# Kernel tuning notes

Hardware: AMD Instinct MI355X
Metric: run time of the kernel (lower is better)

Reference implementation:

```python
import jax, jax.numpy as jnp
import numpy as np

HID = 2048      # hidden_size
NH = 16         # num_attention_heads
QLR = 1536      # q_lora_rank
KVLR = 512      # kv_lora_rank
DN = 128        # qk_nope_head_dim
DR = 64         # qk_rope_head_dim
DQK = DN + DR   # qk_head_dim = 192
DV = 128        # v_head_dim
EPS = 1e-6
THETA = 10000.0
B, T = 2, 2048


def rmsnorm(x, scale):
    return x * jax.lax.rsqrt(jnp.mean(x * x, axis=-1, keepdims=True) + EPS) * scale


def rope(x, positions):
    # x: [B, T, h, d]; NeoX-style rotate-half RoPE on the rope slice only
    d = x.shape[-1]
    inv_freq = 1.0 / (THETA ** (jnp.arange(0, d, 2, dtype=jnp.float32) / d))
    ang = positions.astype(jnp.float32)[..., None] * inv_freq       # [B, T, d/2]
    cos = jnp.cos(ang)[:, :, None, :]
    sin = jnp.sin(ang)[:, :, None, :]
    x1, x2 = jnp.split(x, 2, axis=-1)
    return jnp.concatenate([x1 * cos - x2 * sin, x2 * cos + x1 * sin], axis=-1).astype(x.dtype)


def setup_inputs() -> dict:
    key = jax.random.key(0)
    ks = jax.random.split(key, 8)
    s = 0.02
    x = jax.random.normal(ks[0], (B, T, HID), dtype=jnp.float32)
    attention_mask = jnp.ones((B, T), dtype=bool)
    positions = jnp.broadcast_to(jnp.arange(T, dtype=jnp.int32), (B, T))
    wqa = jax.random.normal(ks[1], (HID, QLR), dtype=jnp.float32) * s
    qa_scale = jnp.ones((QLR,), dtype=jnp.float32)
    wqb = jax.random.normal(ks[2], (QLR, NH * DQK), dtype=jnp.float32) * s
    wkva = jax.random.normal(ks[3], (HID, KVLR + DR), dtype=jnp.float32) * s
    kva_scale = jnp.ones((KVLR,), dtype=jnp.float32)
    wkvb = jax.random.normal(ks[4], (KVLR, NH * (DN + DV)), dtype=jnp.float32) * s
    wo = jax.random.normal(ks[5], (NH * DV, HID), dtype=jnp.float32) * s
    return {"x": x, "attention_mask": attention_mask, "positions": positions,
            "wqa": wqa, "qa_scale": qa_scale, "wqb": wqb,
            "wkva": wkva, "kva_scale": kva_scale, "wkvb": wkvb, "wo": wo}


def reference(x, attention_mask, positions, wqa, qa_scale, wqb, wkva, kva_scale, wkvb, wo):
    Bv, Tv, _ = x.shape
    # low-rank Q: hid -> q_lora_rank -> rmsnorm -> heads*qk_head_dim
    q = (rmsnorm(x @ wqa, qa_scale) @ wqb).reshape(Bv, Tv, NH, DQK)
    q_pass, q_rot = q[..., :DN], q[..., DN:]
    # compressed KV + shared rope key
    ckv = x @ wkva                                    # [B, T, KVLR + DR]
    kv_lat, k_rot = ckv[..., :KVLR], ckv[..., KVLR:].reshape(Bv, Tv, 1, DR)
    kv = (rmsnorm(kv_lat, kva_scale) @ wkvb).reshape(Bv, Tv, NH, DN + DV)
    k_pass, v = kv[..., :DN], kv[..., DN:]
    # decoupled RoPE on rope slice only
    q_rot = rope(q_rot, positions)
    k_rot = jnp.broadcast_to(rope(k_rot, positions), (Bv, Tv, NH, DR))
    q = jnp.concatenate([q_pass, q_rot], axis=-1)     # [B, T, H, 192]
    k = jnp.concatenate([k_pass, k_rot], axis=-1)
    # masked causal SDPA; v padding in the original is a no-op mathematically
    scale = DQK ** -0.5
    scores = jnp.einsum('bqhd,bkhd->bhqk', q, k) * scale
    causal = jnp.tril(jnp.ones((Tv, Tv), dtype=bool))
    mask = causal[None, None, :, :] & attention_mask[:, None, None, :].astype(bool)
    scores = jnp.where(mask, scores, jnp.finfo(scores.dtype).min)
    probs = jax.nn.softmax(scores, axis=-1)
    out = jnp.einsum('bhqk,bkhd->bqhd', probs, v).reshape(Bv, Tv, NH * DV)
    return out @ wo
```

## Files before the change

kernel.cpp:

```cpp
#include <hip/hip_runtime.h>
#include <math.h>
#include <stdint.h>

#define NHEAD 16
#define HIDDIM 2048
#define QLRANK 1536
#define KVRANK 512
#define DROT 64
#define BB 2
#define TT 2048
#define BTOK (BB*TT)
#define NPROJ 2176
#define CKV0 1536
#define ROT0 2048

typedef __bf16 bf16x8 __attribute__((ext_vector_type(8)));
typedef __bf16 bf16x4 __attribute__((ext_vector_type(4)));
typedef float f32x4 __attribute__((ext_vector_type(4)));
typedef uint16_t u16;

__device__ __forceinline__ u16 f2bf(float f) {
  union { float f; uint32_t u; } v; v.f = f;
  uint32_t r = v.u + 0x7fffu + ((v.u >> 16) & 1u);
  return (u16)(r >> 16);
}
__device__ __forceinline__ float bf2f(u16 h) {
  union { uint32_t u; float f; } v; v.u = ((uint32_t)h) << 16;
  return v.f;
}

__device__ __forceinline__ void gload_lds16(const u16* g, u16* l) {
  __builtin_amdgcn_global_load_lds(
      (const __attribute__((address_space(1))) uint32_t*)g,
      (__attribute__((address_space(3))) uint32_t*)l, 16, 0, 0);
}

__global__ __launch_bounds__(256) void cvt_f32_bf16(const float* __restrict__ in,
                                                    u16* __restrict__ out, int n) {
  int idx = (blockIdx.x * 256 + threadIdx.x) * 8;
  if (idx >= n) return;
  f32x4 a = *(const f32x4*)&in[idx];
  f32x4 b = *(const f32x4*)&in[idx + 4];
  union { f32x4 q; u16 e[8]; } w;
#pragma unroll
  for (int j = 0; j < 4; ++j) { w.e[j] = f2bf(a[j]); w.e[4 + j] = f2bf(b[j]); }
  *(f32x4*)&out[idx] = w.q;
}

__global__ __launch_bounds__(256) void transpose_w(const float* __restrict__ W,
                                                   u16* __restrict__ Wt,
                                                   int K, int N, int Npad, float scale,
                                                   const float* __restrict__ svec) {
  __shared__ float tile[32][33];
  int k0 = blockIdx.x * 32, n0 = blockIdx.y * 32;
  int tx = threadIdx.x, ty = threadIdx.y;
#pragma unroll
  for (int r = 0; r < 32; r += 8) {
    int k = k0 + ty + r, n = n0 + tx;
    tile[ty + r][tx] = (k < K && n < N) ? W[(size_t)k * N + n] : 0.f;
  }
  __syncthreads();
  float sv = scale * (svec ? svec[k0 + tx] : 1.f);
#pragma unroll
  for (int r = 0; r < 32; r += 8) {
    int n = n0 + ty + r, k = k0 + tx;
    if (n < Npad && k < K) Wt[(size_t)n * K + k] = f2bf(tile[tx][ty + r] * sv);
  }
}

template<int D>
__global__ __launch_bounds__(256) void row_invrms(const u16* __restrict__ in, int stride,
                                                  float* __restrict__ out) {
  const int row = blockIdx.x;
  const int tid = threadIdx.x;
  constexpr int NC = D / 8;
  float ss = 0.f;
  if (tid < NC) {
    union { f32x4 q; u16 e[8]; } t;
    t.q = *(const f32x4*)&in[(size_t)row * stride + tid * 8];
#pragma unroll
    for (int j = 0; j < 8; ++j) { float v = bf2f(t.e[j]); ss += v * v; }
  }
#pragma unroll
  for (int off = 1; off < 64; off <<= 1) ss += __shfl_xor(ss, off);
  __shared__ float red[4];
  if ((tid & 63) == 0) red[tid >> 6] = ss;
  __syncthreads();
  if (tid == 0)
    out[row] = rsqrtf((red[0] + red[1] + red[2] + red[3]) / (float)D + 1e-6f);
}

template<int OUTF32>
__global__ __launch_bounds__(256) void gemm_bt(const u16* __restrict__ A, int lda,
                                               const u16* __restrict__ Bt,
                                               void* __restrict__ Cv, int ldc,
                                               const float* __restrict__ rowscale,
                                               int N, int K) {
  __shared__ __align__(16) u16 As[2][128 * 32];
  __shared__ __align__(16) u16 Bs[2][128 * 32];
  const int tid = threadIdx.x;
  const int lane = tid & 63;
  const int wave = tid >> 6;
  const int bm = blockIdx.y * 128;
  const int bn = blockIdx.x * 128;
  const int wr = wave >> 1;
  const int wc = wave & 1;

  f32x4 acc[4][4] = {};

  const int srow = wave * 16 + (lane >> 2);
  const int scol = (lane & 3) * 8;
  const u16* Ag = A + (size_t)(bm + srow) * lda + scol;
  const u16* Bg = Bt + (size_t)(bn + srow) * K + scol;
  const int soff = (wave * 16) * 32;

  const int a_off = (wr * 64 + (lane & 15)) * 32 + (lane >> 4) * 8;
  const int b_off = (wc * 64 + (lane & 15)) * 32 + (lane >> 4) * 8;

  const int nt = K >> 5;

  gload_lds16(Ag, &As[0][soff]);
  gload_lds16(Ag + (size_t)64 * lda, &As[0][soff + 64 * 32]);
  gload_lds16(Bg, &Bs[0][soff]);
  gload_lds16(Bg + (size_t)64 * K, &Bs[0][soff + 64 * 32]);
  __syncthreads();

  int cur = 0;
  for (int t = 0; t < nt; ++t) {
    if (t + 1 < nt) {
      const int k0 = (t + 1) << 5;
      gload_lds16(Ag + k0, &As[cur ^ 1][soff]);
      gload_lds16(Ag + (size_t)64 * lda + k0, &As[cur ^ 1][soff + 64 * 32]);
      gload_lds16(Bg + k0, &Bs[cur ^ 1][soff]);
      gload_lds16(Bg + (size_t)64 * K + k0, &Bs[cur ^ 1][soff + 64 * 32]);
    }
    bf16x8 af[4], bfr[4];
#pragma unroll
    for (int m = 0; m < 4; ++m) af[m] = *(const bf16x8*)&As[cur][a_off + m * 16 * 32];
#pragma unroll
    for (int n = 0; n < 4; ++n) bfr[n] = *(const bf16x8*)&Bs[cur][b_off + n * 16 * 32];
#pragma unroll
    for (int m = 0; m < 4; ++m)
#pragma unroll
      for (int n = 0; n < 4; ++n)
        acc[m][n] = __builtin_amdgcn_mfma_f32_16x16x32_bf16(af[m], bfr[n], acc[m][n], 0, 0, 0);
    if (t + 1 < nt) {
      __syncthreads();
      cur ^= 1;
    }
  }

  const int row0 = bm + wr * 64 + (lane >> 4) * 4;
  const int col0 = bn + wc * 64 + (lane & 15);
#pragma unroll
  for (int m = 0; m < 4; ++m) {
    float rs[4] = {1.f, 1.f, 1.f, 1.f};
    if (rowscale) {
#pragma unroll
      for (int i = 0; i < 4; ++i) rs[i] = rowscale[row0 + m * 16 + i];
    }
#pragma unroll
    for (int n = 0; n < 4; ++n)
#pragma unroll
      for (int i = 0; i < 4; ++i) {
        size_t idx = (size_t)(row0 + m * 16 + i) * ldc + (col0 + n * 16);
        float v = acc[m][n][i] * rs[i];
        if (OUTF32) ((float*)Cv)[idx] = v;
        else        ((u16*)Cv)[idx] = f2bf(v);
      }
  }
}

__global__ __launch_bounds__(256) void rope_table(const int* __restrict__ positions,
                                                  float2* __restrict__ tab) {
  int idx = blockIdx.x * 256 + threadIdx.x;
  if (idx >= BTOK * 32) return;
  int bt = idx >> 5, i = idx & 31;
  float invf = powf(10000.0f, -(float)i / 32.0f);
  float ang = (float)positions[bt] * invf;
  tab[idx] = make_float2(cosf(ang), sinf(ang));
}

__global__ __launch_bounds__(256) void rope_q(u16* __restrict__ q,
                                              const float2* __restrict__ tab) {
  int idx = blockIdx.x * 256 + threadIdx.x;
  if (idx >= BTOK * NHEAD * 32) return;
  int i = idx & 31;
  int h = (idx >> 5) & 15;
  int bt = idx >> 9;
  u16* p = q + (size_t)bt * 3072 + h * 192 + 128;
  float x1 = bf2f(p[i]), x2 = bf2f(p[32 + i]);
  float2 cs = tab[bt * 32 + i];
  p[i] = f2bf(x1 * cs.x - x2 * cs.y);
  p[32 + i] = f2bf(x2 * cs.x + x1 * cs.y);
}

__global__ __launch_bounds__(256) void assemble_k(const u16* __restrict__ kv,
                                                  const u16* __restrict__ proj,
                                                  const float2* __restrict__ tab,
                                                  u16* __restrict__ kf) {
  int bt = blockIdx.x;
  __shared__ __align__(16) u16 krot[64];
  int t = threadIdx.x;
  if (t < 64) {
    int i = t & 31;
    float2 cs = tab[bt * 32 + i];
    float x1 = bf2f(proj[(size_t)bt * NPROJ + ROT0 + i]);
    float x2 = bf2f(proj[(size_t)bt * NPROJ + ROT0 + 32 + i]);
    krot[t] = f2bf((t < 32) ? (x1 * cs.x - x2 * cs.y) : (x2 * cs.x + x1 * cs.y));
  }
  __syncthreads();
  for (int c = t; c < 16 * 24; c += 256) {
    int h = c / 24, seg = c % 24;
    u16* dst = kf + (size_t)bt * 3072 + h * 192 + seg * 8;
    if (seg < 16)
      *(f32x4*)dst = *(const f32x4*)&kv[(size_t)bt * 4096 + h * 256 + seg * 8];
    else
      *(f32x4*)dst = *(const f32x4*)&krot[(seg - 16) * 8];
  }
}

__device__ const int8_t JOB_QT[24] = {15,15,7,14,14,13,13,6,12,12,11,11,5,10,10,9,9,4,8,8,3,2,1,0};
__device__ const int8_t JOB_PC[24] = { 0, 1,2, 0, 1, 0, 1,2, 0, 1, 0, 1,2, 0, 1,0,1,2,0,1,2,2,2,2};

__global__ __launch_bounds__(256, 2) void attn_fwd3(const u16* __restrict__ Q,
                                                    const u16* __restrict__ Kf,
                                                    const u16* __restrict__ KV,
                                                    u16* __restrict__ O,
                                                    u16* __restrict__ Opart,
                                                    float2* __restrict__ ml) {
  __shared__ __align__(16) u16 Ks[64 * 192];
  __shared__ __align__(16) u16 Vs[64 * 128];
  __shared__ __align__(16) u16 Ps[4][32][72];

  const int tid = threadIdx.x, lane = tid & 63, wave = tid >> 6;
  const int l15 = lane & 15, l4 = lane >> 4;
  const int jobrank = blockIdx.x >> 5;
  const int bh = blockIdx.x & 31;
  const int qt = JOB_QT[jobrank];
  const int piece = JOB_PC[jobrank];
  const int q0 = qt * 128;
  const int b = bh >> 4, h = bh & 15;
  const int wq0 = q0 + wave * 32;

  bf16x8 qf[2][6];
#pragma unroll
  for (int m = 0; m < 2; ++m) {
    const u16* qp = Q + (size_t)(b * TT + wq0 + m * 16 + l15) * 3072 + h * 192 + l4 * 8;
#pragma unroll
    for (int kk = 0; kk < 6; ++kk) qf[m][kk] = *(const bf16x8*)(qp + kk * 32);
  }

  int ksrc[6];
#pragma unroll
  for (int j = 0; j < 6; ++j) {
    int o = (wave * 6 + j) * 1024 + lane * 16;
    int row = o / 384, col = o % 384;
    int scol = col ^ ((row & 7) << 4);
    ksrc[j] = row * 3072 + (scol >> 1);
  }
  int vsrc[4];
#pragma unroll
  for (int j = 0; j < 4; ++j) {
    int lam = (wave * 4 + j) * 512 + lane * 8;
    int kap = ((lam >> 6) & 15) * 4 + ((lam >> 4) & 3);
    int key = (kap & 3) * 16 + (kap >> 5) * 8 + ((kap >> 2) & 7);
    int dv  = (lam >> 10) * 16 + (lam & 15);
    vsrc[j] = key * 4096 + dv;
  }
  const u16* Kbase = Kf + (size_t)(b * TT) * 3072 + h * 192;
  const u16* Vbase = KV + (size_t)(b * TT) * 4096 + h * 256 + 128;
  u16* KsW = Ks + (wave * 6) * 512;
  u16* VsW = Vs + (wave * 4) * 512;
  const unsigned vs_base = (unsigned)(uintptr_t)(&Vs[0]);

  f32x4 o_acc[2][8] = {};
  float m_r[2][4], l_r[2][4];
#pragma unroll
  for (int m = 0; m < 2; ++m)
#pragma unroll
    for (int i = 0; i < 4; ++i) { m_r[m][i] = -INFINITY; l_r[m][i] = 0.f; }

  const int kt0 = (piece == 1) ? (qt + 1) : 0;
  const int kt1 = (piece == 0) ? (qt + 1) : (2 * qt + 2);

  for (int kt = kt0; kt < kt1; ++kt) {
    __syncthreads();
    const u16* Kt = Kbase + (size_t)(kt * 64) * 3072;
    const u16* Vt = Vbase + (size_t)(kt * 64) * 4096;
#pragma unroll
    for (int j = 0; j < 6; ++j) gload_lds16(Kt + ksrc[j], KsW + j * 512);
#pragma unroll
    for (int j = 0; j < 4; ++j) gload_lds16(Vt + vsrc[j], VsW + j * 512);
    __syncthreads();

    if (kt * 64 > wq0 + 31) continue;

    f32x4 s[2][4] = {};
#pragma unroll
    for (int n = 0; n < 4; ++n) {
      const int krow = n * 16 + l15;
      const int swz = (l15 & 7) << 3;
#pragma unroll
      for (int kk = 0; kk < 6; ++kk) {
        bf16x8 kb = *(const bf16x8*)&Ks[krow * 192 + ((kk * 32 + l4 * 8) ^ swz)];
        s[0][n] = __builtin_amdgcn_mfma_f32_16x16x32_bf16(qf[0][kk], kb, s[0][n], 0, 0, 0);
        s[1][n] = __builtin_amdgcn_mfma_f32_16x16x32_bf16(qf[1][kk], kb, s[1][n], 0, 0, 0);
      }
    }

    const bool needmask = (kt * 64 + 63) > wq0;
    const int pbase = (l15 >> 3) * 32 + (l15 & 3) * 8 + ((l15 >> 2) & 1) * 4;
#pragma unroll
    for (int m = 0; m < 2; ++m) {
      float sv[4][4], pmax[4], alpha[4];
      const int qrow0 = wq0 + m * 16 + l4 * 4;
#pragma unroll
      for (int i = 0; i < 4; ++i) pmax[i] = -INFINITY;
#pragma unroll
      for (int n = 0; n < 4; ++n)
#pragma unroll
        for (int i = 0; i < 4; ++i) {
          float v = s[m][n][i];
          if (needmask && (kt * 64 + n * 16 + l15 > qrow0 + i)) v = -INFINITY;
          sv[n][i] = v;
          pmax[i] = fmaxf(pmax[i], v);
        }
#pragma unroll
      for (int i = 0; i < 4; ++i) {
#pragma unroll
        for (int off = 1; off < 16; off <<= 1) pmax[i] = fmaxf(pmax[i], __shfl_xor(pmax[i], off));
        float mn = fmaxf(m_r[m][i], pmax[i]);
        alpha[i] = __expf(m_r[m][i] - mn);
        m_r[m][i] = mn;
      }
      float psum[4] = {0.f, 0.f, 0.f, 0.f};
#pragma unroll
      for (int i = 0; i < 4; ++i) {
        union { uint2 d; u16 e[4]; } pk;
#pragma unroll
        for (int n = 0; n < 4; ++n) {
          float p = __expf(sv[n][i] - m_r[m][i]);
          psum[i] += p;
          pk.e[n] = f2bf(p);
        }
        *(uint2*)&Ps[wave][m * 16 + l4 * 4 + i][pbase] = pk.d;
      }
#pragma unroll
      for (int i = 0; i < 4; ++i) {
#pragma unroll
        for (int off = 1; off < 16; off <<= 1) psum[i] += __shfl_xor(psum[i], off);
        l_r[m][i] = l_r[m][i] * alpha[i] + psum[i];
      }
#pragma unroll
      for (int n = 0; n < 8; ++n)
#pragma unroll
        for (int i = 0; i < 4; ++i) o_acc[m][n][i] *= alpha[i];
    }

    asm volatile("s_waitcnt lgkmcnt(0)" ::: "memory");
    __builtin_amdgcn_sched_barrier(0);

#pragma unroll
    for (int kk = 0; kk < 2; ++kk) {
      bf16x8 pa0 = *(const bf16x8*)&Ps[wave][l15][kk * 32 + l4 * 8];
      bf16x8 pa1 = *(const bf16x8*)&Ps[wave][16 + l15][kk * 32 + l4 * 8];
      const unsigned va = vs_base + kk * 1024 + lane * 8;
#pragma unroll
      for (int g = 0; g < 2; ++g) {
        union { uint2 u; bf16x4 b; } lo[4], hi[4];
#pragma unroll
        for (int n = 0; n < 4; ++n) {
          unsigned a0 = va + (g * 4 + n) * 2048;
          asm volatile("ds_read_b64_tr_b16 %0, %1" : "=v"(lo[n].u) : "v"(a0));
          asm volatile("ds_read_b64_tr_b16 %0, %1 offset:512" : "=v"(hi[n].u) : "v"(a0));
        }
        asm volatile("s_waitcnt lgkmcnt(0)" ::: "memory");
        __builtin_amdgcn_sched_barrier(0);
#pragma unroll
        for (int n = 0; n < 4; ++n) {
          bf16x8 vb = __builtin_shufflevector(lo[n].b, hi[n].b, 0, 1, 2, 3, 4, 5, 6, 7);
          o_acc[0][g * 4 + n] = __builtin_amdgcn_mfma_f32_16x16x32_bf16(pa0, vb, o_acc[0][g * 4 + n], 0, 0, 0);
          o_acc[1][g * 4 + n] = __builtin_amdgcn_mfma_f32_16x16x32_bf16(pa1, vb, o_acc[1][g * 4 + n], 0, 0, 0);
        }
      }
    }
  }

  if (piece == 2) {
    float l_inv[2][4];
#pragma unroll
    for (int m = 0; m < 2; ++m)
#pragma unroll
      for (int i = 0; i < 4; ++i) l_inv[m][i] = 1.f / l_r[m][i];
#pragma unroll
    for (int m = 0; m < 2; ++m)
#pragma unroll
      for (int n = 0; n < 8; ++n)
#pragma unroll
        for (int i = 0; i < 4; ++i) {
          int r = q0 + wave * 32 + m * 16 + l4 * 4 + i;
          O[(size_t)(b * TT + r) * 2048 + h * 128 + n * 16 + l15] = f2bf(o_acc[m][n][i] * l_inv[m][i]);
        }
  } else {
    const size_t pidx = ((size_t)(qt - 8) * 32 + bh) * 2 + piece;
    u16* op = Opart + pidx * (128 * 128);
    float2* mlp = ml + pidx * 128;
#pragma unroll
    for (int m = 0; m < 2; ++m)
#pragma unroll
      for (int n = 0; n < 8; ++n)
#pragma unroll
        for (int i = 0; i < 4; ++i)
          op[(wave * 32 + m * 16 + l4 * 4 + i) * 128 + n * 16 + l15] = f2bf(o_acc[m][n][i]);
    if (l15 == 0) {
#pragma unroll
      for (int m = 0; m < 2; ++m)
#pragma unroll
        for (int i = 0; i < 4; ++i)
          mlp[wave * 32 + m * 16 + l4 * 4 + i] = make_float2(m_r[m][i], l_r[m][i]);
    }
  }
}

__global__ __launch_bounds__(256) void attn_combine(const u16* __restrict__ Opart,
                                                    const float2* __restrict__ ml,
                                                    u16* __restrict__ O) {
  int gid = blockIdx.x * 256 + threadIdx.x;
  int dvseg = gid & 15;
  int row = (gid >> 4) & 127;
  int bh = (gid >> 11) & 31;
  int qt8 = gid >> 16;
  size_t i1 = ((size_t)qt8 * 32 + bh) * 2;
  float2 ml1 = ml[i1 * 128 + row], ml2 = ml[(i1 + 1) * 128 + row];
  float m = fmaxf(ml1.x, ml2.x);
  float w1 = __expf(ml1.x - m), w2 = __expf(ml2.x - m);
  float inv = 1.f / (w1 * ml1.y + w2 * ml2.y);
  union { f32x4 q; u16 e[8]; } a, bq, w;
  a.q  = *(const f32x4*)&Opart[i1 * 16384 + row * 128 + dvseg * 8];
  bq.q = *(const f32x4*)&Opart[(i1 + 1) * 16384 + row * 128 + dvseg * 8];
#pragma unroll
  for (int j = 0; j < 8; ++j)
    w.e[j] = f2bf((w1 * bf2f(a.e[j]) + w2 * bf2f(bq.e[j])) * inv);
  int b = bh >> 4, h = bh & 15;
  int r = 1024 + qt8 * 128 + row;
  *(f32x4*)&O[(size_t)(b * TT + r) * 2048 + h * 128 + dvseg * 8] = w.q;
}

extern "C" void kernel_launch(void* const* d_in, const int* in_sizes, int n_in,
                              void* d_out, int out_size, void* d_ws, size_t ws_size,
                              hipStream_t stream) {
  (void)in_sizes; (void)n_in; (void)out_size; (void)ws_size;
  const float* x         = (const float*)d_in[0];
  const int*   positions = (const int*)d_in[2];
  const float* wqa       = (const float*)d_in[3];
  const float* qa_scale  = (const float*)d_in[4];
  const float* wqb       = (const float*)d_in[5];
  const float* wkva      = (const float*)d_in[6];
  const float* kva_scale = (const float*)d_in[7];
  const float* wkvb      = (const float*)d_in[8];
  const float* wo        = (const float*)d_in[9];
  float* out = (float*)d_out;

  char* wsp = (char*)d_ws;
  auto alloc = [&](size_t bytes) {
    char* p = wsp; wsp += (bytes + 255) & ~(size_t)255; return p;
  };
  u16* xb      = (u16*)alloc((size_t)BTOK * HIDDIM * 2);
  u16* proj_t  = (u16*)alloc((size_t)NPROJ * HIDDIM * 2);
  u16* wqb_t   = (u16*)alloc((size_t)3072 * QLRANK * 2);
  u16* wkvb_t  = (u16*)alloc((size_t)4096 * KVRANK * 2);
  u16* wo_t    = (u16*)alloc((size_t)HIDDIM * HIDDIM * 2);
  u16* proj    = (u16*)alloc((size_t)BTOK * NPROJ * 2);
  u16* q       = (u16*)alloc((size_t)BTOK * 3072 * 2);
  u16* kv      = (u16*)alloc((size_t)BTOK * 4096 * 2);
  u16* kf      = (u16*)alloc((size_t)BTOK * 3072 * 2);
  float2* tab  = (float2*)alloc((size_t)BTOK * 32 * 8);
  float* invq  = (float*)alloc((size_t)BTOK * 4);
  float* invkv = (float*)alloc((size_t)BTOK * 4);
  float2* mlbuf= (float2*)alloc((size_t)8 * 32 * 2 * 128 * 8);
  u16* ao = xb;
  u16* Opart = proj;

  dim3 blk(256);
  const float qscale = 0.07216878364870322f;

  cvt_f32_bf16<<<(BTOK * HIDDIM / 8 + 255) / 256, blk, 0, stream>>>(x, xb, BTOK * HIDDIM);
  {
    dim3 tb(32, 8);
    transpose_w<<<dim3(HIDDIM / 32, QLRANK / 32), tb, 0, stream>>>(wqa, proj_t, HIDDIM, QLRANK, QLRANK, 1.f, nullptr);
    transpose_w<<<dim3(HIDDIM / 32, (NPROJ - CKV0) / 32), tb, 0, stream>>>(wkva, proj_t + (size_t)CKV0 * HIDDIM, HIDDIM, 576, NPROJ - CKV0, 1.f, nullptr);
    transpose_w<<<dim3(QLRANK / 32, 3072 / 32), tb, 0, stream>>>(wqb, wqb_t, QLRANK, 3072, 3072, qscale, qa_scale);
    transpose_w<<<dim3(KVRANK / 32, 4096 / 32), tb, 0, stream>>>(wkvb, wkvb_t, KVRANK, 4096, 4096, 1.f, kva_scale);
    transpose_w<<<dim3(HIDDIM / 32, HIDDIM / 32), tb, 0, stream>>>(wo, wo_t, HIDDIM, HIDDIM, HIDDIM, 1.f, nullptr);
  }
  rope_table<<<(BTOK * 32 + 255) / 256, blk, 0, stream>>>(positions, tab);

  gemm_bt<0><<<dim3(NPROJ / 128, BTOK / 128), blk, 0, stream>>>(xb, HIDDIM, proj_t, proj, NPROJ, nullptr, NPROJ, HIDDIM);

  row_invrms<QLRANK><<<BTOK, blk, 0, stream>>>(proj, NPROJ, invq);
  row_invrms<KVRANK><<<BTOK, blk, 0, stream>>>(proj + CKV0, NPROJ, invkv);

  gemm_bt<0><<<dim3(3072 / 128, BTOK / 128), blk, 0, stream>>>(proj, NPROJ, wqb_t, q, 3072, invq, 3072, QLRANK);
  gemm_bt<0><<<dim3(4096 / 128, BTOK / 128), blk, 0, stream>>>(proj + CKV0, NPROJ, wkvb_t, kv, 4096, invkv, 4096, KVRANK);

  rope_q<<<(BTOK * NHEAD * 32 + 255) / 256, blk, 0, stream>>>(q, tab);
  assemble_k<<<BTOK, blk, 0, stream>>>(kv, proj, tab, kf);

  attn_fwd3<<<dim3(24 * 32), blk, 0, stream>>>(q, kf, kv, ao, Opart, mlbuf);
  attn_combine<<<(8 * 32 * 128 * 16) / 256, blk, 0, stream>>>(Opart, mlbuf, ao);

  gemm_bt<1><<<dim3(HIDDIM / 128, BTOK / 128), blk, 0, stream>>>(ao, HIDDIM, wo_t, out, HIDDIM, nullptr, HIDDIM, HIDDIM);
}
```

Measured before the change: 375.2 us.

## Compute transposed scores to keep P in registers and skip rescale via threshold

The attention kernel now computes S^T (K as the A operand), so each lane holds one query row's scores. Row max and sum need only two cross-lane shuffles, and the P tile is built with register shuffles instead of a round trip through LDS. The V permutation is changed to match the new P layout. Dropping the Ps buffer lets the launch bound rise to 3 blocks per CU. The kernel also skips the online-softmax rescale when the max grows by at most 8, in the style of FA4, which risks larger exponent values but stays exact after normalisation. s_setprio is raised around the MFMA sections.

Result: slower. 497.2 us (+32.5%).

```diff
diff --git a/kernel.cpp b/kernel.cpp
--- a/kernel.cpp
+++ b/kernel.cpp
@@ -18,6 +18,7 @@
 typedef __bf16 bf16x4 __attribute__((ext_vector_type(4)));
 typedef float f32x4 __attribute__((ext_vector_type(4)));
 typedef uint16_t u16;
+typedef uint32_t u32;
 
 __device__ __forceinline__ u16 f2bf(float f) {
   union { float f; uint32_t u; } v; v.f = f;
@@ -223,7 +224,7 @@
 __device__ const int8_t JOB_QT[24] = {15,15,7,14,14,13,13,6,12,12,11,11,5,10,10,9,9,4,8,8,3,2,1,0};
 __device__ const int8_t JOB_PC[24] = { 0, 1,2, 0, 1, 0, 1,2, 0, 1, 0, 1,2, 0, 1,0,1,2,0,1,2,2,2,2};
 
-__global__ __launch_bounds__(256, 2) void attn_fwd3(const u16* __restrict__ Q,
+__global__ __launch_bounds__(256, 3) void attn_fwd4(const u16* __restrict__ Q,
                                                     const u16* __restrict__ Kf,
                                                     const u16* __restrict__ KV,
                                                     u16* __restrict__ O,
@@ -231,7 +232,6 @@
                                                     float2* __restrict__ ml) {
   __shared__ __align__(16) u16 Ks[64 * 192];
   __shared__ __align__(16) u16 Vs[64 * 128];
-  __shared__ __align__(16) u16 Ps[4][32][72];
 
   const int tid = threadIdx.x, lane = tid & 63, wave = tid >> 6;
   const int l15 = lane & 15, l4 = lane >> 4;
@@ -264,7 +264,7 @@
   for (int j = 0; j < 4; ++j) {
     int lam = (wave * 4 + j) * 512 + lane * 8;
     int kap = ((lam >> 6) & 15) * 4 + ((lam >> 4) & 3);
-    int key = (kap & 3) * 16 + (kap >> 5) * 8 + ((kap >> 2) & 7);
+    int key = ((kap >> 5) & 1) * 32 + ((kap >> 2) & 3) * 8 + ((kap >> 4) & 1) * 4 + (kap & 3);
     int dv  = (lam >> 10) * 16 + (lam & 15);
     vsrc[j] = key * 4096 + dv;
   }
@@ -275,11 +275,9 @@
   const unsigned vs_base = (unsigned)(uintptr_t)(&Vs[0]);
 
   f32x4 o_acc[2][8] = {};
-  float m_r[2][4], l_r[2][4];
-#pragma unroll
-  for (int m = 0; m < 2; ++m)
-#pragma unroll
-    for (int i = 0; i < 4; ++i) { m_r[m][i] = -INFINITY; l_r[m][i] = 0.f; }
+  float m_r[2], l_r[2];
+#pragma unroll
+  for (int m = 0; m < 2; ++m) { m_r[m] = -INFINITY; l_r[m] = 0.f; }
 
   const int kt0 = (piece == 1) ? (qt + 1) : 0;
   const int kt1 = (piece == 0) ? (qt + 1) : (2 * qt + 2);
@@ -295,8 +293,10 @@
     __syncthreads();
 
     if (kt * 64 > wq0 + 31) continue;
+    const int kt64 = kt * 64;
 
     f32x4 s[2][4] = {};
+    __builtin_amdgcn_s_setprio(1);
 #pragma unroll
     for (int n = 0; n < 4; ++n) {
       const int krow = n * 16 + l15;
@@ -304,67 +304,80 @@
 #pragma unroll
       for (int kk = 0; kk < 6; ++kk) {
         bf16x8 kb = *(const bf16x8*)&Ks[krow * 192 + ((kk * 32 + l4 * 8) ^ swz)];
-        s[0][n] = __builtin_amdgcn_mfma_f32_16x16x32_bf16(qf[0][kk], kb, s[0][n], 0, 0, 0);
-        s[1][n] = __builtin_amdgcn_mfma_f32_16x16x32_bf16(qf[1][kk], kb, s[1][n], 0, 0, 0);
-      }
-    }
-
-    const bool needmask = (kt * 64 + 63) > wq0;
-    const int pbase = (l15 >> 3) * 32 + (l15 & 3) * 8 + ((l15 >> 2) & 1) * 4;
+        s[0][n] = __builtin_amdgcn_mfma_f32_16x16x32_bf16(kb, qf[0][kk], s[0][n], 0, 0, 0);
+        s[1][n] = __builtin_amdgcn_mfma_f32_16x16x32_bf16(kb, qf[1][kk], s[1][n], 0, 0, 0);
+      }
+    }
+    __builtin_amdgcn_s_setprio(0);
+
+    u32 pk[2][4][2];
 #pragma unroll
     for (int m = 0; m < 2; ++m) {
-      float sv[4][4], pmax[4], alpha[4];
-      const int qrow0 = wq0 + m * 16 + l4 * 4;
-#pragma unroll
-      for (int i = 0; i < 4; ++i) pmax[i] = -INFINITY;
+      const int qrow = wq0 + m * 16 + l15;
+      const bool needmask = (kt64 + 63) > (wq0 + m * 16);
+      if (needmask) {
+#pragma unroll
+        for (int n = 0; n < 4; ++n)
+#pragma unroll
+          for (int i = 0; i < 4; ++i)
+            if (kt64 + n * 16 + l4 * 4 + i > qrow) s[m][n][i] = -INFINITY;
+      }
+      float pmax = -INFINITY;
 #pragma unroll
       for (int n = 0; n < 4; ++n)
 #pragma unroll
-        for (int i = 0; i < 4; ++i) {
-          float v = s[m][n][i];
-          if (needmask && (kt * 64 + n * 16 + l15 > qrow0 + i)) v = -INFINITY;
-          sv[n][i] = v;
-          pmax[i] = fmaxf(pmax[i], v);
+        for (int i = 0; i < 4; ++i) pmax = fmaxf(pmax, s[m][n][i]);
+      pmax = fmaxf(pmax, __shfl_xor(pmax, 16));
+      pmax = fmaxf(pmax, __shfl_xor(pmax, 32));
+
+      if (!__all(pmax - m_r[m] <= 8.f)) {
+        float mn = fmaxf(m_r[m], pmax);
+        float alpha = __expf(m_r[m] - mn);
+        m_r[m] = mn;
+        l_r[m] *= alpha;
+        float ab[4];
+#pragma unroll
+        for (int i = 0; i < 4; ++i) ab[i] = __shfl(alpha, l4 * 4 + i);
+#pragma unroll
+        for (int n = 0; n < 8; ++n)
+#pragma unroll
+          for (int i = 0; i < 4; ++i) o_acc[m][n][i] *= ab[i];
+      }
+
+      float psum = 0.f;
+#pragma unroll
+      for (int n = 0; n < 4; ++n) {
+        float p0 = __expf(s[m][n][0] - m_r[m]);
+        float p1 = __expf(s[m][n][1] - m_r[m]);
+        float p2 = __expf(s[m][n][2] - m_r[m]);
+        float p3 = __expf(s[m][n][3] - m_r[m]);
+        psum += (p0 + p1) + (p2 + p3);
+        union { u32 u; __bf16 e[2]; } a, c;
+        a.e[0] = (__bf16)p0; a.e[1] = (__bf16)p1;
+        c.e[0] = (__bf16)p2; c.e[1] = (__bf16)p3;
+        pk[m][n][0] = a.u;
+        pk[m][n][1] = c.u;
+      }
+      psum += __shfl_xor(psum, 16);
+      psum += __shfl_xor(psum, 32);
+      l_r[m] += psum;
+    }
+
+#pragma unroll
+    for (int kk = 0; kk < 2; ++kk) {
+      bf16x8 pa[2];
+#pragma unroll
+      for (int m = 0; m < 2; ++m) {
+        union { u32 w[4]; bf16x8 v; } uu;
+#pragma unroll
+        for (int t = 0; t < 4; ++t) {
+          int src = l15 + ((2 * (l4 & 1) + (t >> 1)) << 4);
+          u32 a0 = __shfl(pk[m][2 * kk + 0][t & 1], src);
+          u32 a1 = __shfl(pk[m][2 * kk + 1][t & 1], src);
+          uu.w[t] = (l4 & 2) ? a1 : a0;
         }
-#pragma unroll
-      for (int i = 0; i < 4; ++i) {
-#pragma unroll
-        for (int off = 1; off < 16; off <<= 1) pmax[i] = fmaxf(pmax[i], __shfl_xor(pmax[i], off));
-        float mn = fmaxf(m_r[m][i], pmax[i]);
-        alpha[i] = __expf(m_r[m][i] - mn);
-        m_r[m][i] = mn;
-      }
-      float psum[4] = {0.f, 0.f, 0.f, 0.f};
-#pragma unroll
-      for (int i = 0; i < 4; ++i) {
-        union { uint2 d; u16 e[4]; } pk;
-#pragma unroll
-        for (int n = 0; n < 4; ++n) {
-          float p = __expf(sv[n][i] - m_r[m][i]);
-          psum[i] += p;
-          pk.e[n] = f2bf(p);
-        }
-        *(uint2*)&Ps[wave][m * 16 + l4 * 4 + i][pbase] = pk.d;
-      }
-#pragma unroll
-      for (int i = 0; i < 4; ++i) {
-#pragma unroll
-        for (int off = 1; off < 16; off <<= 1) psum[i] += __shfl_xor(psum[i], off);
-        l_r[m][i] = l_r[m][i] * alpha[i] + psum[i];
-      }
-#pragma unroll
-      for (int n = 0; n < 8; ++n)
-#pragma unroll
-        for (int i = 0; i < 4; ++i) o_acc[m][n][i] *= alpha[i];
-    }
-
-    asm volatile("s_waitcnt lgkmcnt(0)" ::: "memory");
-    __builtin_amdgcn_sched_barrier(0);
-
-#pragma unroll
-    for (int kk = 0; kk < 2; ++kk) {
-      bf16x8 pa0 = *(const bf16x8*)&Ps[wave][l15][kk * 32 + l4 * 8];
-      bf16x8 pa1 = *(const bf16x8*)&Ps[wave][16 + l15][kk * 32 + l4 * 8];
+        pa[m] = uu.v;
+      }
       const unsigned va = vs_base + kk * 1024 + lane * 8;
 #pragma unroll
       for (int g = 0; g < 2; ++g) {
@@ -377,31 +390,33 @@
         }
         asm volatile("s_waitcnt lgkmcnt(0)" ::: "memory");
         __builtin_amdgcn_sched_barrier(0);
+        __builtin_amdgcn_s_setprio(1);
 #pragma unroll
         for (int n = 0; n < 4; ++n) {
           bf16x8 vb = __builtin_shufflevector(lo[n].b, hi[n].b, 0, 1, 2, 3, 4, 5, 6, 7);
-          o_acc[0][g * 4 + n] = __builtin_amdgcn_mfma_f32_16x16x32_bf16(pa0, vb, o_acc[0][g * 4 + n], 0, 0, 0);
-          o_acc[1][g * 4 + n] = __builtin_amdgcn_mfma_f32_16x16x32_bf16(pa1, vb, o_acc[1][g * 4 + n], 0, 0, 0);
+          o_acc[0][g * 4 + n] = __builtin_amdgcn_mfma_f32_16x16x32_bf16(pa[0], vb, o_acc[0][g * 4 + n], 0, 0, 0);
+          o_acc[1][g * 4 + n] = __builtin_amdgcn_mfma_f32_16x16x32_bf16(pa[1], vb, o_acc[1][g * 4 + n], 0, 0, 0);
         }
+        __builtin_amdgcn_s_setprio(0);
       }
     }
   }
 
   if (piece == 2) {
-    float l_inv[2][4];
-#pragma unroll
-    for (int m = 0; m < 2; ++m)
-#pragma unroll
-      for (int i = 0; i < 4; ++i) l_inv[m][i] = 1.f / l_r[m][i];
-#pragma unroll
-    for (int m = 0; m < 2; ++m)
+#pragma unroll
+    for (int m = 0; m < 2; ++m) {
+      float inv = 1.f / l_r[m];
+      float li[4];
+#pragma unroll
+      for (int i = 0; i < 4; ++i) li[i] = __shfl(inv, l4 * 4 + i);
 #pragma unroll
       for (int n = 0; n < 8; ++n)
 #pragma unroll
         for (int i = 0; i < 4; ++i) {
-          int r = q0 + wave * 32 + m * 16 + l4 * 4 + i;
-          O[(size_t)(b * TT + r) * 2048 + h * 128 + n * 16 + l15] = f2bf(o_acc[m][n][i] * l_inv[m][i]);
+          int r = wq0 + m * 16 + l4 * 4 + i;
+          O[(size_t)(b * TT + r) * 2048 + h * 128 + n * 16 + l15] = f2bf(o_acc[m][n][i] * li[i]);
         }
+    }
   } else {
     const size_t pidx = ((size_t)(qt - 8) * 32 + bh) * 2 + piece;
     u16* op = Opart + pidx * (128 * 128);
@@ -413,12 +428,10 @@
 #pragma unroll
         for (int i = 0; i < 4; ++i)
           op[(wave * 32 + m * 16 + l4 * 4 + i) * 128 + n * 16 + l15] = f2bf(o_acc[m][n][i]);
-    if (l15 == 0) {
+    if (l4 == 0) {
 #pragma unroll
       for (int m = 0; m < 2; ++m)
-#pragma unroll
-        for (int i = 0; i < 4; ++i)
-          mlp[wave * 32 + m * 16 + l4 * 4 + i] = make_float2(m_r[m][i], l_r[m][i]);
+        mlp[wave * 32 + m * 16 + l15] = make_float2(m_r[m], l_r[m]);
     }
   }
 }
@@ -507,7 +520,7 @@
   rope_q<<<(BTOK * NHEAD * 32 + 255) / 256, blk, 0, stream>>>(q, tab);
   assemble_k<<<BTOK, blk, 0, stream>>>(kv, proj, tab, kf);
 
-  attn_fwd3<<<dim3(24 * 32), blk, 0, stream>>>(q, kf, kv, ao, Opart, mlbuf);
+  attn_fwd4<<<dim3(24 * 32), blk, 0, stream>>>(q, kf, kv, ao, Opart, mlbuf);
   attn_combine<<<(8 * 32 * 128 * 16) / 256, blk, 0, stream>>>(Opart, mlbuf, ao);
 
   gemm_bt<1><<<dim3(HIDDIM / 128, BTOK / 128), blk, 0, stream>>>(ao, HIDDIM, wo_t, out, HIDDIM, nullptr, HIDDIM, HIDDIM);
```
